# Performance work log

Measured on AMD Instinct MI355X. Metric: run time of the kernel, lower is better.

Reference implementation:

```python
import jax, jax.numpy as jnp
import numpy as np

GROUPS = 32
EPS = 1e-6


def group_norm(h, scale, bias):
    B, C, H, W = h.shape
    hg = h.reshape(B, GROUPS, -1)
    mu = hg.mean(axis=-1, keepdims=True)
    var = hg.var(axis=-1, keepdims=True)
    hg = (hg - mu) * jax.lax.rsqrt(var + EPS)
    h = hg.reshape(B, C, H, W)
    return h * scale[None, :, None, None] + bias[None, :, None, None]


def conv1x1(h, W, b):
    # 1x1 conv == per-pixel linear: (B,C,H,W) x (O,C) -> (B,O,H,W)
    return jnp.einsum('bchw,oc->bohw', h, W) + b[None, :, None, None]


def setup_inputs() -> dict:
    key = jax.random.key(0)
    ks = jax.random.split(key, 6)
    B, C, H, W = 8, 512, 64, 64
    s = 0.02
    return {
        'x': jax.random.normal(ks[0], (B, C, H, W), jnp.float32),
        'gn_scale': jnp.ones((C,), jnp.float32),
        'gn_bias': jnp.zeros((C,), jnp.float32),
        'Wq': jax.random.normal(ks[1], (C, C), jnp.float32) * s,
        'bq': jnp.zeros((C,), jnp.float32),
        'Wk': jax.random.normal(ks[2], (C, C), jnp.float32) * s,
        'bk': jnp.zeros((C,), jnp.float32),
        'Wv': jax.random.normal(ks[3], (C, C), jnp.float32) * s,
        'bv': jnp.zeros((C,), jnp.float32),
        'Wo': jax.random.normal(ks[4], (C, C), jnp.float32) * s,
        'bo': jnp.zeros((C,), jnp.float32),
    }


def reference(x, gn_scale, gn_bias, Wq, bq, Wk, bk, Wv, bv, Wo, bo):
    B, C, H, W = x.shape
    N = H * W
    h = group_norm(x, gn_scale, gn_bias)
    q = conv1x1(h, Wq, bq).reshape(B, C, N)   # (B,C,N)
    k = conv1x1(h, Wk, bk).reshape(B, C, N)
    v = conv1x1(h, Wv, bv).reshape(B, C, N)
    # scores: q^T k, scaled by C^-0.5
    w = jnp.einsum('bcq,bck->bqk', q, k) * (C ** -0.5)  # (B,N_q,N_k)
    w = jax.nn.softmax(w, axis=-1)
    # h = v @ w^T  -> (B,C,N_q)
    h = jnp.einsum('bck,bqk->bcq', v, w).reshape(B, C, H, W)
    h = conv1x1(h, Wo, bo)
    return x + h
```

## Files before the change

kernel.cpp:

```cpp
#include <hip/hip_runtime.h>
#include <math.h>

typedef __bf16 bf16_t;
typedef __bf16 bf8v __attribute__((ext_vector_type(8)));
typedef __bf16 bf4v __attribute__((ext_vector_type(4)));
typedef float  f4v  __attribute__((ext_vector_type(4)));

#define BB  8
#define CC  512
#define NN  4096
#define CPG 16
#define NCb (NN * CC)
#define WSZ (CC * CC)

#define FLG_SIZES 805306368.f
#define FLG_WS    536870912.f

__global__ void diag_out(float* out, float v) { if (threadIdx.x == 0) out[0] = v; }

__device__ __forceinline__ void gload_lds16(const bf16_t* g, bf16_t* l)
{
    __builtin_amdgcn_global_load_lds(
        (const __attribute__((address_space(1))) unsigned int*)g,
        (__attribute__((address_space(3))) unsigned int*)l, 16, 0, 0);
}

__global__ __launch_bounds__(256) void cvt_w(const float* __restrict__ a,
                                             const float* __restrict__ b,
                                             const float* __restrict__ c,
                                             const float* __restrict__ d,
                                             bf16_t* __restrict__ o)
{
    const int i = (blockIdx.x * 256 + threadIdx.x) * 4;
    const float* srcs[4] = {a, b, c, d};
#pragma unroll
    for (int m = 0; m < 4; m++) {
        float4 v = *(const float4*)(srcs[m] + i);
        bf4v w;
        w[0] = (bf16_t)v.x; w[1] = (bf16_t)v.y;
        w[2] = (bf16_t)v.z; w[3] = (bf16_t)v.w;
        *(bf4v*)(o + (size_t)m * WSZ + i) = w;
    }
}

__global__ __launch_bounds__(256) void gn_stats_part(const float* __restrict__ x,
                                                     double* __restrict__ part)
{
    const int bg = blockIdx.x >> 2;
    const int sl = blockIdx.x & 3;
    const int tid = threadIdx.x;
    const float4* xv = (const float4*)(x + (size_t)bg * CPG * NN) + sl * 4096;
    double s[4] = {0, 0, 0, 0}, ss[4] = {0, 0, 0, 0};
#pragma unroll
    for (int ii = 0; ii < 16; ii++) {
        float4 v = xv[tid + ii * 256];
        const int a = ii & 3;
        s[a]  += (double)v.x + (double)v.y + (double)v.z + (double)v.w;
        ss[a] += (double)v.x * v.x + (double)v.y * v.y
               + (double)v.z * v.z + (double)v.w * v.w;
    }
    double sT = s[0] + s[1] + s[2] + s[3];
    double ssT = ss[0] + ss[1] + ss[2] + ss[3];
    __shared__ double l1[256], l2[256];
    l1[tid] = sT; l2[tid] = ssT;
    __syncthreads();
    for (int o = 128; o > 0; o >>= 1) {
        if (tid < o) { l1[tid] += l1[tid + o]; l2[tid] += l2[tid + o]; }
        __syncthreads();
    }
    if (tid == 0) {
        part[(size_t)blockIdx.x * 2]     = l1[0];
        part[(size_t)blockIdx.x * 2 + 1] = l2[0];
    }
}

__global__ __launch_bounds__(256) void gn_stats_fin(const double* __restrict__ part,
                                                    float* __restrict__ stats)
{
    const int bg = threadIdx.x;
    double s = 0.0, ss = 0.0;
#pragma unroll
    for (int sl = 0; sl < 4; sl++) {
        s  += part[(size_t)(bg * 4 + sl) * 2];
        ss += part[(size_t)(bg * 4 + sl) * 2 + 1];
    }
    double mean = s * (1.0 / 65536.0);
    double var  = ss * (1.0 / 65536.0) - mean * mean;
    stats[bg * 2]     = (float)mean;
    stats[bg * 2 + 1] = (float)(1.0 / sqrt(var + 1e-6));
}

__global__ __launch_bounds__(256) void gn_apply_all(const float* __restrict__ x,
                                                    const float* __restrict__ gw,
                                                    const float* __restrict__ gb,
                                                    const float* __restrict__ stats,
                                                    bf16_t* __restrict__ h_all)
{
    const int b  = blockIdx.y;
    const int g  = blockIdx.x >> 4;
    const int sl = blockIdx.x & 15;
    const float* xp = x + (size_t)b * CC * NN + (size_t)g * CPG * NN;
    bf16_t* h = h_all + (size_t)b * NCb;
    const int tid = threadIdx.x;
    const float mean = stats[(b * 32 + g) * 2];
    const float rstd = stats[(b * 32 + g) * 2 + 1];
    const int cw = tid & 15;
    const float aa = rstd * gw[g * CPG + cw];
    const float bb = gb[g * CPG + cw] - mean * aa;

    __shared__ float tile[CPG][260];
    const int n0 = sl * 256;
    for (int i = tid; i < (CPG * 256) / 4; i += 256) {
        int c  = i >> 6;
        int n4 = i & 63;
        float4 v = *(const float4*)(xp + (size_t)c * NN + n0 + n4 * 4);
        tile[c][n4 * 4 + 0] = v.x;
        tile[c][n4 * 4 + 1] = v.y;
        tile[c][n4 * 4 + 2] = v.z;
        tile[c][n4 * 4 + 3] = v.w;
    }
    __syncthreads();
#pragma unroll
    for (int j = 0; j < 16; j++) {
        int n = (tid >> 4) + 16 * j;
        float v = tile[cw][n] * aa + bb;
        h[(size_t)(n0 + n) * CC + g * CPG + cw] = (bf16_t)v;
    }
}

__global__ __launch_bounds__(256) void gn_apply(const float* __restrict__ xb,
                                                const float* __restrict__ gw,
                                                const float* __restrict__ gb,
                                                const float* __restrict__ stats,
                                                bf16_t* __restrict__ h,
                                                int bg0)
{
    const int g  = blockIdx.x >> 4;
    const int sl = blockIdx.x & 15;
    const float* xp = xb + (size_t)g * CPG * NN;
    const int tid = threadIdx.x;
    const float mean = stats[(bg0 + g) * 2];
    const float rstd = stats[(bg0 + g) * 2 + 1];
    const int cw = tid & 15;
    const float aa = rstd * gw[g * CPG + cw];
    const float bb = gb[g * CPG + cw] - mean * aa;

    __shared__ float tile[CPG][260];
    const int n0 = sl * 256;
    for (int i = tid; i < (CPG * 256) / 4; i += 256) {
        int c  = i >> 6;
        int n4 = i & 63;
        float4 v = *(const float4*)(xp + (size_t)c * NN + n0 + n4 * 4);
        tile[c][n4 * 4 + 0] = v.x;
        tile[c][n4 * 4 + 1] = v.y;
        tile[c][n4 * 4 + 2] = v.z;
        tile[c][n4 * 4 + 3] = v.w;
    }
    __syncthreads();
#pragma unroll
    for (int j = 0; j < 16; j++) {
        int n = (tid >> 4) + 16 * j;
        float v = tile[cw][n] * aa + bb;
        h[(size_t)(n0 + n) * CC + g * CPG + cw] = (bf16_t)v;
    }
}

#define ABUF (128 * 32)
#define BBUF (256 * 32)

__device__ __forceinline__ void gemm_core_w(
    const bf16_t* __restrict__ A, const bf16_t* __restrict__ B,
    int K, int lda, int ldb, size_t m0, size_t n0,
    bf16_t* Asm, bf16_t* Bsm,
    int wave, int lane, int wm, int wn, int fr, int fq, f4v acc[4][8])
{
    const int gr = lane >> 2;
    const int gc = (lane & 3) << 3;
    const bf16_t* pa = A + (m0 + wave * 32 + gr) * lda + gc;
    const bf16_t* pb = B + (n0 + wave * 64 + gr) * ldb + gc;
    const int la0 = (wave * 32) * 32;
    const int lb0 = (wave * 64) * 32;

    {
        bf16_t* lA = Asm + la0;
        bf16_t* lB = Bsm + lb0;
        gload_lds16(pa,                     lA);
        gload_lds16(pa + (size_t)16 * lda,  lA + 16 * 32);
        gload_lds16(pb,                     lB);
        gload_lds16(pb + (size_t)16 * ldb,  lB + 16 * 32);
        gload_lds16(pb + (size_t)32 * ldb,  lB + 32 * 32);
        gload_lds16(pb + (size_t)48 * ldb,  lB + 48 * 32);
    }

    int buf = 0;
    for (int kt = 0; kt < K; kt += 32) {
        if (kt + 32 < K) {
            const int nb = buf ^ 1;
            bf16_t* lA = Asm + nb * ABUF + la0;
            bf16_t* lB = Bsm + nb * BBUF + lb0;
            const int kn = kt + 32;
            gload_lds16(pa + kn,                     lA);
            gload_lds16(pa + kn + (size_t)16 * lda,  lA + 16 * 32);
            gload_lds16(pb + kn,                     lB);
            gload_lds16(pb + kn + (size_t)16 * ldb,  lB + 16 * 32);
            gload_lds16(pb + kn + (size_t)32 * ldb,  lB + 32 * 32);
            gload_lds16(pb + kn + (size_t)48 * ldb,  lB + 48 * 32);
            asm volatile("s_waitcnt vmcnt(6)" ::: "memory");
        } else {
            asm volatile("s_waitcnt vmcnt(0)" ::: "memory");
        }
        __builtin_amdgcn_s_barrier();

        const bf16_t* As = Asm + buf * ABUF;
        const bf16_t* Bs = Bsm + buf * BBUF;
        bf8v af[4], bfv[8];
#pragma unroll
        for (int j = 0; j < 8; j++)
            bfv[j] = *(const bf8v*)(Bs + (wn + j * 16 + fr) * 32 + fq * 8);
#pragma unroll
        for (int i = 0; i < 4; i++)
            af[i] = *(const bf8v*)(As + (wm + i * 16 + fr) * 32 + fq * 8);
#pragma unroll
        for (int i = 0; i < 4; i++)
#pragma unroll
            for (int j = 0; j < 8; j++)
                acc[i][j] = __builtin_amdgcn_mfma_f32_16x16x32_bf16(
                    af[i], bfv[j], acc[i][j], 0, 0, 0);

        __builtin_amdgcn_s_barrier();
        buf ^= 1;
    }
}

template <int MODE>
__global__ __launch_bounds__(256, 2) void gemm_bt(
    const bf16_t* __restrict__ A, const bf16_t* __restrict__ B,
    void* __restrict__ Og, const float* __restrict__ bias,
    const float* __restrict__ resid, float scale,
    int K, int lda, int ldb, int ldo)
{
    __shared__ bf16_t Asm[2 * ABUF];
    __shared__ bf16_t Bsm[2 * BBUF];
    const int tid  = threadIdx.x;
    const int lane = tid & 63, wave = tid >> 6;
    const int wm = (wave >> 1) << 6, wn = (wave & 1) << 7;
    const int fr = lane & 15, fq = lane >> 4;
    const size_t m0 = (size_t)blockIdx.x * 128, n0 = (size_t)blockIdx.y * 256;

    f4v acc[4][8];
#pragma unroll
    for (int i = 0; i < 4; i++)
#pragma unroll
        for (int j = 0; j < 8; j++) acc[i][j] = (f4v){0.f, 0.f, 0.f, 0.f};

    gemm_core_w(A, B, K, lda, ldb, m0, n0, Asm, Bsm,
                wave, lane, wm, wn, fr, fq, acc);

    if (MODE == 0) {
        bf16_t* out = (bf16_t*)Og;
#pragma unroll
        for (int i = 0; i < 4; i++) {
            const int mb = (int)m0 + wm + i * 16 + fq * 4;
#pragma unroll
            for (int j = 0; j < 8; j++) {
                const int n = (int)n0 + wn + j * 16 + fr;
                const float bn = bias ? bias[n] : 0.f;
#pragma unroll
                for (int t = 0; t < 4; t++)
                    out[(size_t)(mb + t) * ldo + n] =
                        (bf16_t)(acc[i][j][t] * scale + bn);
            }
        }
    } else {
        float* out = (float*)Og;
#pragma unroll
        for (int i = 0; i < 4; i++) {
            const int mb = (int)m0 + wm + i * 16 + fq * 4;
#pragma unroll
            for (int j = 0; j < 8; j++) {
                const int n = (int)n0 + wn + j * 16 + fr;
                const float bn = bias[n];
                float4 rq = *(const float4*)(resid + (size_t)n * ldo + mb);
                float4 o4;
                o4.x = acc[i][j][0] * scale + bn + rq.x;
                o4.y = acc[i][j][1] * scale + bn + rq.y;
                o4.z = acc[i][j][2] * scale + bn + rq.z;
                o4.w = acc[i][j][3] * scale + bn + rq.w;
                *(float4*)(out + (size_t)n * ldo + mb) = o4;
            }
        }
    }
}

__global__ __launch_bounds__(256, 2) void gemm_qkt(
    const bf16_t* __restrict__ q_all, const bf16_t* __restrict__ k_all,
    bf16_t* __restrict__ S2, int bp, float scale)
{
    __shared__ bf16_t Asm[2 * ABUF];
    __shared__ bf16_t Bsm[2 * BBUF];
    const int z = blockIdx.z;
    const bf16_t* A = q_all + (size_t)(bp + z) * NCb;
    const bf16_t* B = k_all + (size_t)(bp + z) * NCb;
    bf16_t* out = S2 + (size_t)z * NN * NN;

    const int tid  = threadIdx.x;
    const int lane = tid & 63, wave = tid >> 6;
    const int wm = (wave >> 1) << 6, wn = (wave & 1) << 7;
    const int fr = lane & 15, fq = lane >> 4;
    const size_t m0 = (size_t)blockIdx.x * 128, n0 = (size_t)blockIdx.y * 256;

    f4v acc[4][8];
#pragma unroll
    for (int i = 0; i < 4; i++)
#pragma unroll
        for (int j = 0; j < 8; j++) acc[i][j] = (f4v){0.f, 0.f, 0.f, 0.f};

    gemm_core_w(A, B, 512, 512, 512, m0, n0, Asm, Bsm,
                wave, lane, wm, wn, fr, fq, acc);

#pragma unroll
    for (int i = 0; i < 4; i++) {
        const int mb = (int)m0 + wm + i * 16 + fq * 4;
#pragma unroll
        for (int j = 0; j < 8; j++) {
            const int n = (int)n0 + wn + j * 16 + fr;
#pragma unroll
            for (int t = 0; t < 4; t++)
                out[(size_t)(mb + t) * NN + n] = (bf16_t)(acc[i][j][t] * scale);
        }
    }
}

__global__ __launch_bounds__(256, 2) void gemm_pv2(
    const bf16_t* __restrict__ S2, const bf16_t* __restrict__ v_all,
    float* __restrict__ P, int bp)
{
    __shared__ bf16_t Asm[2 * ABUF];
    __shared__ bf16_t Bsm[2 * BBUF];
    const int slot = blockIdx.z >> 2;
    const int s    = blockIdx.z & 3;
    const int k0   = s * 1024;
    const bf16_t* A = S2 + (size_t)slot * NN * NN + k0;
    const bf16_t* B = v_all + (size_t)(bp + slot) * NCb + k0;
    float* out = P + ((size_t)slot * 4 + s) * NCb;

    const int tid  = threadIdx.x;
    const int lane = tid & 63, wave = tid >> 6;
    const int wm = (wave >> 1) << 6, wn = (wave & 1) << 7;
    const int fr = lane & 15, fq = lane >> 4;
    const size_t m0 = (size_t)blockIdx.x * 128, n0 = (size_t)blockIdx.y * 256;

    f4v acc[4][8];
#pragma unroll
    for (int i = 0; i < 4; i++)
#pragma unroll
        for (int j = 0; j < 8; j++) acc[i][j] = (f4v){0.f, 0.f, 0.f, 0.f};

    gemm_core_w(A, B, 1024, NN, NN, m0, n0, Asm, Bsm,
                wave, lane, wm, wn, fr, fq, acc);

#pragma unroll
    for (int i = 0; i < 4; i++) {
        const int mb = (int)m0 + wm + i * 16 + fq * 4;
#pragma unroll
        for (int j = 0; j < 8; j++) {
            const int n = (int)n0 + wn + j * 16 + fr;
#pragma unroll
            for (int t = 0; t < 4; t++)
                out[(size_t)(mb + t) * CC + n] = acc[i][j][t];
        }
    }
}

__global__ __launch_bounds__(256) void pv_reduce2(const float* __restrict__ P,
                                                  bf16_t* __restrict__ O_all,
                                                  int bp)
{
    const int slot = blockIdx.y;
    const size_t i = ((size_t)blockIdx.x * 256 + threadIdx.x) * 4;
    const float* Ps = P + (size_t)slot * 4 * NCb;
    float4 sv = *(const float4*)(Ps + i);
#pragma unroll
    for (int z = 1; z < 4; z++) {
        float4 t = *(const float4*)(Ps + (size_t)z * NCb + i);
        sv.x += t.x; sv.y += t.y; sv.z += t.z; sv.w += t.w;
    }
    bf4v o;
    o[0] = (bf16_t)sv.x; o[1] = (bf16_t)sv.y;
    o[2] = (bf16_t)sv.z; o[3] = (bf16_t)sv.w;
    *(bf4v*)(O_all + (size_t)(bp + slot) * NCb + i) = o;
}

__global__ __launch_bounds__(256, 2) void gemm_pv_split(
    const bf16_t* __restrict__ A, const bf16_t* __restrict__ B,
    float* __restrict__ P, int KS)
{
    __shared__ bf16_t Asm[2 * ABUF];
    __shared__ bf16_t Bsm[2 * BBUF];
    const int tid  = threadIdx.x;
    const int lane = tid & 63, wave = tid >> 6;
    const int wm = (wave >> 1) << 6, wn = (wave & 1) << 7;
    const int fr = lane & 15, fq = lane >> 4;
    const size_t m0 = (size_t)blockIdx.x * 128, n0 = (size_t)blockIdx.y * 256;
    const int z  = blockIdx.z;
    const int k0 = z * KS;

    f4v acc[4][8];
#pragma unroll
    for (int i = 0; i < 4; i++)
#pragma unroll
        for (int j = 0; j < 8; j++) acc[i][j] = (f4v){0.f, 0.f, 0.f, 0.f};

    gemm_core_w(A + k0, B + k0, KS, NN, NN, m0, n0, Asm, Bsm,
                wave, lane, wm, wn, fr, fq, acc);

    float* out = P + (size_t)z * NCb;
#pragma unroll
    for (int i = 0; i < 4; i++) {
        const int mb = (int)m0 + wm + i * 16 + fq * 4;
#pragma unroll
        for (int j = 0; j < 8; j++) {
            const int n = (int)n0 + wn + j * 16 + fr;
#pragma unroll
            for (int t = 0; t < 4; t++)
                out[(size_t)(mb + t) * CC + n] = acc[i][j][t];
        }
    }
}

__global__ __launch_bounds__(256) void pv_reduce(const float* __restrict__ P,
                                                 bf16_t* __restrict__ O, int NS)
{
    const size_t i = ((size_t)blockIdx.x * 256 + threadIdx.x) * 4;
    float4 s = *(const float4*)(P + i);
    for (int z = 1; z < NS; z++) {
        float4 t = *(const float4*)(P + (size_t)z * NCb + i);
        s.x += t.x; s.y += t.y; s.z += t.z; s.w += t.w;
    }
    bf4v o;
    o[0] = (bf16_t)s.x; o[1] = (bf16_t)s.y;
    o[2] = (bf16_t)s.z; o[3] = (bf16_t)s.w;
    *(bf4v*)(O + i) = o;
}

__global__ __launch_bounds__(256, 2) void gemm_out_all(
    const bf16_t* __restrict__ Oall, const bf16_t* __restrict__ Wo,
    float* __restrict__ outg, const float* __restrict__ bo,
    const float* __restrict__ x)
{
    __shared__ bf16_t Asm[2 * ABUF];
    __shared__ bf16_t Bsm[2 * BBUF];
    const int b = blockIdx.z;
    const bf16_t* A = Oall + (size_t)b * NCb;
    float* out = outg + (size_t)b * CC * NN;
    const float* resid = x + (size_t)b * CC * NN;

    const int tid  = threadIdx.x;
    const int lane = tid & 63, wave = tid >> 6;
    const int wm = (wave >> 1) << 6, wn = (wave & 1) << 7;
    const int fr = lane & 15, fq = lane >> 4;
    const size_t m0 = (size_t)blockIdx.x * 128, n0 = (size_t)blockIdx.y * 256;

    f4v acc[4][8];
#pragma unroll
    for (int i = 0; i < 4; i++)
#pragma unroll
        for (int j = 0; j < 8; j++) acc[i][j] = (f4v){0.f, 0.f, 0.f, 0.f};

    gemm_core_w(A, Wo, 512, 512, 512, m0, n0, Asm, Bsm,
                wave, lane, wm, wn, fr, fq, acc);

#pragma unroll
    for (int i = 0; i < 4; i++) {
        const int mb = (int)m0 + wm + i * 16 + fq * 4;
#pragma unroll
        for (int j = 0; j < 8; j++) {
            const int n = (int)n0 + wn + j * 16 + fr;
            const float bn = bo[n];
            float4 rq = *(const float4*)(resid + (size_t)n * NN + mb);
            float4 o4;
            o4.x = acc[i][j][0] + bn + rq.x;
            o4.y = acc[i][j][1] + bn + rq.y;
            o4.z = acc[i][j][2] + bn + rq.z;
            o4.w = acc[i][j][3] + bn + rq.w;
            *(float4*)(out + (size_t)n * NN + mb) = o4;
        }
    }
}

__global__ __launch_bounds__(256, 2) void gemm_qkv_all(
    const bf16_t* __restrict__ h_all, const bf16_t* __restrict__ Wb,
    const float* __restrict__ bq, const float* __restrict__ bk,
    const float* __restrict__ bv,
    bf16_t* __restrict__ q_all, bf16_t* __restrict__ k_all,
    bf16_t* __restrict__ v_all)
{
    __shared__ bf16_t Asm[2 * ABUF];
    __shared__ bf16_t Bsm[2 * BBUF];
    const int sel = blockIdx.z >> 3;
    const int b   = blockIdx.z & 7;
    const bf16_t* h = h_all + (size_t)b * NCb;
    const bf16_t* B = Wb + (size_t)sel * WSZ;
    const float* bias = (sel == 0) ? bq : (sel == 1) ? bk : bv;
    bf16_t* out = ((sel == 0) ? q_all : (sel == 1) ? k_all : v_all)
                + (size_t)b * NCb;

    const int tid  = threadIdx.x;
    const int lane = tid & 63, wave = tid >> 6;
    const int wm = (wave >> 1) << 6, wn = (wave & 1) << 7;
    const int fr = lane & 15, fq = lane >> 4;
    const size_t m0 = (size_t)blockIdx.x * 128, n0 = (size_t)blockIdx.y * 256;

    f4v acc[4][8];
#pragma unroll
    for (int i = 0; i < 4; i++)
#pragma unroll
        for (int j = 0; j < 8; j++) acc[i][j] = (f4v){0.f, 0.f, 0.f, 0.f};

    gemm_core_w(h, B, 512, 512, 512, m0, n0, Asm, Bsm,
                wave, lane, wm, wn, fr, fq, acc);

    if (sel < 2) {
#pragma unroll
        for (int i = 0; i < 4; i++) {
            const int mb = (int)m0 + wm + i * 16 + fq * 4;
#pragma unroll
            for (int j = 0; j < 8; j++) {
                const int n = (int)n0 + wn + j * 16 + fr;
                const float bn = bias[n];
#pragma unroll
                for (int t = 0; t < 4; t++)
                    out[(size_t)(mb + t) * 512 + n] =
                        (bf16_t)(acc[i][j][t] + bn);
            }
        }
    } else {
#pragma unroll
        for (int i = 0; i < 4; i++) {
            const int mb = (int)m0 + wm + i * 16 + fq * 4;
#pragma unroll
            for (int j = 0; j < 8; j++) {
                const int n = (int)n0 + wn + j * 16 + fr;
                const float bn = bias[n];
                bf4v pk;
#pragma unroll
                for (int t = 0; t < 4; t++)
                    pk[t] = (bf16_t)(acc[i][j][t] + bn);
                *(bf4v*)(out + (size_t)n * NN + mb) = pk;
            }
        }
    }
}

__global__ __launch_bounds__(256, 2) void gemm_qkv(
    const bf16_t* __restrict__ h, const bf16_t* __restrict__ Wb,
    const float* __restrict__ bq, const float* __restrict__ bk,
    const float* __restrict__ bv,
    bf16_t* __restrict__ q, bf16_t* __restrict__ k, bf16_t* __restrict__ v)
{
    __shared__ bf16_t Asm[2 * ABUF];
    __shared__ bf16_t Bsm[2 * BBUF];
    const int z = blockIdx.z;
    const bf16_t* B = Wb + (size_t)z * WSZ;
    const float* bias = (z == 0) ? bq : (z == 1) ? bk : bv;
    bf16_t* out = (z == 0) ? q : (z == 1) ? k : v;

    const int tid  = threadIdx.x;
    const int lane = tid & 63, wave = tid >> 6;
    const int wm = (wave >> 1) << 6, wn = (wave & 1) << 7;
    const int fr = lane & 15, fq = lane >> 4;
    const size_t m0 = (size_t)blockIdx.x * 128, n0 = (size_t)blockIdx.y * 256;

    f4v acc[4][8];
#pragma unroll
    for (int i = 0; i < 4; i++)
#pragma unroll
        for (int j = 0; j < 8; j++) acc[i][j] = (f4v){0.f, 0.f, 0.f, 0.f};

    gemm_core_w(h, B, 512, 512, 512, m0, n0, Asm, Bsm,
                wave, lane, wm, wn, fr, fq, acc);

    if (z < 2) {
#pragma unroll
        for (int i = 0; i < 4; i++) {
            const int mb = (int)m0 + wm + i * 16 + fq * 4;
#pragma unroll
            for (int j = 0; j < 8; j++) {
                const int n = (int)n0 + wn + j * 16 + fr;
                const float bn = bias[n];
#pragma unroll
                for (int t = 0; t < 4; t++)
                    out[(size_t)(mb + t) * 512 + n] =
                        (bf16_t)(acc[i][j][t] + bn);
            }
        }
    } else {
#pragma unroll
        for (int i = 0; i < 4; i++) {
            const int mb = (int)m0 + wm + i * 16 + fq * 4;
#pragma unroll
            for (int j = 0; j < 8; j++) {
                const int n = (int)n0 + wn + j * 16 + fr;
                const float bn = bias[n];
                bf4v pk;
#pragma unroll
                for (int t = 0; t < 4; t++)
                    pk[t] = (bf16_t)(acc[i][j][t] + bn);
                *(bf4v*)(out + (size_t)n * NN + mb) = pk;
            }
        }
    }
}

__global__ __launch_bounds__(256) void softmax_kernel(bf16_t* __restrict__ S)
{
    const int wave = threadIdx.x >> 6, lane = threadIdx.x & 63;
    const size_t row = (size_t)blockIdx.x * 4 + wave;
    bf16_t* p = S + row * NN;
    float f[64];
    float mx = -1e30f;
#pragma unroll
    for (int c = 0; c < 8; c++) {
        bf8v v = ((const bf8v*)p)[c * 64 + lane];
#pragma unroll
        for (int j = 0; j < 8; j++) {
            f[c * 8 + j] = (float)v[j];
            mx = fmaxf(mx, f[c * 8 + j]);
        }
    }
#pragma unroll
    for (int off = 32; off > 0; off >>= 1) mx = fmaxf(mx, __shfl_xor(mx, off));
    float sum = 0.f;
#pragma unroll
    for (int i = 0; i < 64; i++) { f[i] = expf(f[i] - mx); sum += f[i]; }
#pragma unroll
    for (int off = 32; off > 0; off >>= 1) sum += __shfl_xor(sum, off);
    const float inv = 1.f / sum;
#pragma unroll
    for (int c = 0; c < 8; c++) {
        bf8v o;
#pragma unroll
        for (int j = 0; j < 8; j++) o[j] = (bf16_t)(f[c * 8 + j] * inv);
        ((bf8v*)p)[c * 64 + lane] = o;
    }
}

extern "C" void kernel_launch(void* const* d_in, const int* in_sizes, int n_in,
                              void* d_out, int out_size, void* d_ws, size_t ws_size,
                              hipStream_t stream)
{
    const float* x  = (const float*)d_in[0];
    const float* gw = (const float*)d_in[1];
    const float* gb = (const float*)d_in[2];
    const float* Wq = (const float*)d_in[3];
    const float* bq = (const float*)d_in[4];
    const float* Wk = (const float*)d_in[5];
    const float* bk = (const float*)d_in[6];
    const float* Wv = (const float*)d_in[7];
    const float* bv = (const float*)d_in[8];
    const float* Wo = (const float*)d_in[9];
    const float* bo = (const float*)d_in[10];
    float* out = (float*)d_out;

    bool ok = (n_in == 11) && (out_size == BB * CC * NN) &&
              (in_sizes[0] == BB * CC * NN) &&
              (in_sizes[1] == CC) && (in_sizes[2] == CC) &&
              (in_sizes[3] == WSZ) && (in_sizes[4] == CC) &&
              (in_sizes[5] == WSZ) && (in_sizes[6] == CC) &&
              (in_sizes[7] == WSZ) && (in_sizes[8] == CC) &&
              (in_sizes[9] == WSZ) && (in_sizes[10] == CC);
    if (!ok) { diag_out<<<dim3(1), 64, 0, stream>>>(out, FLG_SIZES); return; }

    const float sc = 0.044194173824159216f;

    bf16_t* Wb    = (bf16_t*)d_ws;
    float*  stats = (float*)(Wb + (size_t)4 * WSZ);
    double* part  = (double*)(stats + 1024);
    bf16_t* base  = (bf16_t*)(part + 2048);
    const size_t head = (size_t)4 * WSZ * 2 + 1024 * 4 + 2048 * 8;

    const size_t sfull = (size_t)NN * NN * 2;

    cvt_w<<<dim3(256), 256, 0, stream>>>(Wq, Wk, Wv, Wo, Wb);
    gn_stats_part<<<dim3(1024), 256, 0, stream>>>(x, part);
    gn_stats_fin<<<dim3(1), 256, 0, stream>>>(part, stats);

    if (ws_size >= head + (size_t)4 * BB * NCb * 2 + 2 * sfull) {
        bf16_t* h_all = base;
        bf16_t* q_all = h_all + (size_t)BB * NCb;
        bf16_t* k_all = q_all + (size_t)BB * NCb;
        bf16_t* v_all = k_all + (size_t)BB * NCb;
        bf16_t* S2    = v_all + (size_t)BB * NCb;
        float*  P     = out;
        bf16_t* O_all = h_all;

        gn_apply_all<<<dim3(512, 8), 256, 0, stream>>>(x, gw, gb, stats, h_all);
        gemm_qkv_all<<<dim3(32, 2, 24), 256, 0, stream>>>(
            h_all, Wb, bq, bk, bv, q_all, k_all, v_all);

        for (int bp = 0; bp < BB; bp += 2) {
            gemm_qkt<<<dim3(32, 16, 2), 256, 0, stream>>>(
                q_all, k_all, S2, bp, sc);
            softmax_kernel<<<dim3(2 * NN / 4), 256, 0, stream>>>(S2);
            gemm_pv2<<<dim3(32, 2, 8), 256, 0, stream>>>(S2, v_all, P, bp);
            pv_reduce2<<<dim3(NCb / 1024, 2), 256, 0, stream>>>(P, O_all, bp);
        }

        gemm_out_all<<<dim3(32, 2, 8), 256, 0, stream>>>(
            O_all, Wb + (size_t)3 * WSZ, out, bo, x);
        return;
    }

    bf16_t* h = base;
    bf16_t* q = h + (size_t)NCb;
    bf16_t* k = q + (size_t)NCb;
    bf16_t* v = k + (size_t)NCb;
    bf16_t* S = v + (size_t)NCb;
    bf16_t* O = h;
    const size_t fixed = head + (size_t)4 * NCb * 2;

    if (ws_size < fixed + (size_t)128 * NN * 2) {
        diag_out<<<dim3(1), 64, 0, stream>>>(out, FLG_WS); return;
    }

    int NS = 0;
    if (ws_size >= fixed + sfull + (size_t)8 * NCb * 4)      NS = 8;
    else if (ws_size >= fixed + sfull + (size_t)4 * NCb * 4) NS = 4;
    else if (ws_size >= fixed + sfull + (size_t)2 * NCb * 4) NS = 2;

    if (NS) {
        float* P = (float*)(S + (size_t)NN * NN);
        for (int b = 0; b < BB; b++) {
            const float* xb   = x   + (size_t)b * CC * NN;
            float*       outb = out + (size_t)b * CC * NN;

            gn_apply<<<dim3(512), 256, 0, stream>>>(xb, gw, gb, stats, h, b * 32);
            gemm_qkv<<<dim3(32, 2, 3), 256, 0, stream>>>(h, Wb, bq, bk, bv, q, k, v);

            gemm_bt<0><<<dim3(32, 16), 256, 0, stream>>>(
                q, k, S, nullptr, nullptr, sc, 512, 512, 512, 4096);
            softmax_kernel<<<dim3(NN / 4), 256, 0, stream>>>(S);

            gemm_pv_split<<<dim3(32, 2, NS), 256, 0, stream>>>(S, v, P, NN / NS);
            pv_reduce<<<dim3(NCb / 1024), 256, 0, stream>>>(P, O, NS);

            gemm_bt<2><<<dim3(32, 2), 256, 0, stream>>>(
                O, Wb + (size_t)3 * WSZ, outb, bo, xb, 1.f,
                512, 512, 512, 4096);
        }
        return;
    }

    int CH = 128;
    while (CH < NN && fixed + (size_t)(CH * 2) * NN * 2 <= ws_size) CH *= 2;

    for (int b = 0; b < BB; b++) {
        const float* xb   = x   + (size_t)b * CC * NN;
        float*       outb = out + (size_t)b * CC * NN;

        gn_apply<<<dim3(512), 256, 0, stream>>>(xb, gw, gb, stats, h, b * 32);
        gemm_qkv<<<dim3(32, 2, 3), 256, 0, stream>>>(h, Wb, bq, bk, bv, q, k, v);

        for (int r0 = 0; r0 < NN; r0 += CH) {
            gemm_bt<0><<<dim3(CH / 128, 16), 256, 0, stream>>>(
                q + (size_t)r0 * CC, k, S, nullptr, nullptr, sc,
                512, 512, 512, 4096);
            softmax_kernel<<<dim3(CH / 4), 256, 0, stream>>>(S);
            gemm_bt<0><<<dim3(CH / 128, 2), 256, 0, stream>>>(
                S, v, O + (size_t)r0 * CC, nullptr, nullptr, 1.f,
                4096, 4096, 4096, 512);
        }

        gemm_bt<2><<<dim3(32, 2), 256, 0, stream>>>(
            O, Wb + (size_t)3 * WSZ, outb, bo, xb, 1.f,
            512, 512, 512, 4096);
    }
}
```

Before: 806.7 us.

## Triple-buffer GEMM LDS pipeline and XOR-swizzle LDS layout

Moves the shared GEMM core from double to triple buffering, so two K-tiles of global-to-LDS loads are in flight, with vmcnt waits adjusted to match. It also XOR-swizzles the 16-byte column chunk per row on both the global source address and the LDS fragment reads to reduce LDS bank conflicts. LDS per block grows from 48 KB to 72 KB, which may cut occupancy below the two blocks per CU requested in launch bounds.

```diff
diff --git a/kernel.cpp b/kernel.cpp
--- a/kernel.cpp
+++ b/kernel.cpp
@@ -167,6 +167,19 @@
 
 #define ABUF (128 * 32)
 #define BBUF (256 * 32)
+#define NBUF 3
+
+__device__ __forceinline__ void stage_tile(
+    const bf16_t* pa, const bf16_t* pb, int lda, int ldb,
+    bf16_t* lA, bf16_t* lB)
+{
+    gload_lds16(pa,                     lA);
+    gload_lds16(pa + (size_t)16 * lda,  lA + 16 * 32);
+    gload_lds16(pb,                     lB);
+    gload_lds16(pb + (size_t)16 * ldb,  lB + 16 * 32);
+    gload_lds16(pb + (size_t)32 * ldb,  lB + 32 * 32);
+    gload_lds16(pb + (size_t)48 * ldb,  lB + 48 * 32);
+}
 
 __device__ __forceinline__ void gemm_core_w(
     const bf16_t* __restrict__ A, const bf16_t* __restrict__ B,
@@ -174,37 +187,27 @@
     bf16_t* Asm, bf16_t* Bsm,
     int wave, int lane, int wm, int wn, int fr, int fq, f4v acc[4][8])
 {
-    const int gr = lane >> 2;
-    const int gc = (lane & 3) << 3;
-    const bf16_t* pa = A + (m0 + wave * 32 + gr) * lda + gc;
-    const bf16_t* pb = B + (n0 + wave * 64 + gr) * ldb + gc;
+    const int gr  = lane >> 2;
+    const int gcs = (((lane & 3) ^ (gr & 3)) << 3);
+    const bf16_t* pa = A + (m0 + wave * 32 + gr) * lda + gcs;
+    const bf16_t* pb = B + (n0 + wave * 64 + gr) * ldb + gcs;
     const int la0 = (wave * 32) * 32;
     const int lb0 = (wave * 64) * 32;
-
-    {
-        bf16_t* lA = Asm + la0;
-        bf16_t* lB = Bsm + lb0;
-        gload_lds16(pa,                     lA);
-        gload_lds16(pa + (size_t)16 * lda,  lA + 16 * 32);
-        gload_lds16(pb,                     lB);
-        gload_lds16(pb + (size_t)16 * ldb,  lB + 16 * 32);
-        gload_lds16(pb + (size_t)32 * ldb,  lB + 32 * 32);
-        gload_lds16(pb + (size_t)48 * ldb,  lB + 48 * 32);
-    }
+    const int fqs = ((fq ^ (fr & 3)) << 3);
+
+    stage_tile(pa, pb, lda, ldb, Asm + la0, Bsm + lb0);
+    if (K > 32)
+        stage_tile(pa + 32, pb + 32, lda, ldb,
+                   Asm + ABUF + la0, Bsm + BBUF + lb0);
 
     int buf = 0;
     for (int kt = 0; kt < K; kt += 32) {
-        if (kt + 32 < K) {
-            const int nb = buf ^ 1;
-            bf16_t* lA = Asm + nb * ABUF + la0;
-            bf16_t* lB = Bsm + nb * BBUF + lb0;
-            const int kn = kt + 32;
-            gload_lds16(pa + kn,                     lA);
-            gload_lds16(pa + kn + (size_t)16 * lda,  lA + 16 * 32);
-            gload_lds16(pb + kn,                     lB);
-            gload_lds16(pb + kn + (size_t)16 * ldb,  lB + 16 * 32);
-            gload_lds16(pb + kn + (size_t)32 * ldb,  lB + 32 * 32);
-            gload_lds16(pb + kn + (size_t)48 * ldb,  lB + 48 * 32);
+        if (kt + 64 < K) {
+            const int nb = (buf + 2 >= NBUF) ? buf + 2 - NBUF : buf + 2;
+            stage_tile(pa + kt + 64, pb + kt + 64, lda, ldb,
+                       Asm + nb * ABUF + la0, Bsm + nb * BBUF + lb0);
+            asm volatile("s_waitcnt vmcnt(12)" ::: "memory");
+        } else if (kt + 32 < K) {
             asm volatile("s_waitcnt vmcnt(6)" ::: "memory");
         } else {
             asm volatile("s_waitcnt vmcnt(0)" ::: "memory");
@@ -216,10 +219,10 @@
         bf8v af[4], bfv[8];
 #pragma unroll
         for (int j = 0; j < 8; j++)
-            bfv[j] = *(const bf8v*)(Bs + (wn + j * 16 + fr) * 32 + fq * 8);
+            bfv[j] = *(const bf8v*)(Bs + (wn + j * 16 + fr) * 32 + fqs);
 #pragma unroll
         for (int i = 0; i < 4; i++)
-            af[i] = *(const bf8v*)(As + (wm + i * 16 + fr) * 32 + fq * 8);
+            af[i] = *(const bf8v*)(As + (wm + i * 16 + fr) * 32 + fqs);
 #pragma unroll
         for (int i = 0; i < 4; i++)
 #pragma unroll
@@ -228,7 +231,7 @@
                     af[i], bfv[j], acc[i][j], 0, 0, 0);
 
         __builtin_amdgcn_s_barrier();
-        buf ^= 1;
+        buf = (buf + 1 == NBUF) ? 0 : buf + 1;
     }
 }
 
@@ -239,8 +242,8 @@
     const float* __restrict__ resid, float scale,
     int K, int lda, int ldb, int ldo)
 {
-    __shared__ bf16_t Asm[2 * ABUF];
-    __shared__ bf16_t Bsm[2 * BBUF];
+    __shared__ bf16_t Asm[NBUF * ABUF];
+    __shared__ bf16_t Bsm[NBUF * BBUF];
     const int tid  = threadIdx.x;
     const int lane = tid & 63, wave = tid >> 6;
     const int wm = (wave >> 1) << 6, wn = (wave & 1) << 7;
@@ -296,8 +299,8 @@
     const bf16_t* __restrict__ q_all, const bf16_t* __restrict__ k_all,
     bf16_t* __restrict__ S2, int bp, float scale)
 {
-    __shared__ bf16_t Asm[2 * ABUF];
-    __shared__ bf16_t Bsm[2 * BBUF];
+    __shared__ bf16_t Asm[NBUF * ABUF];
+    __shared__ bf16_t Bsm[NBUF * BBUF];
     const int z = blockIdx.z;
     const bf16_t* A = q_all + (size_t)(bp + z) * NCb;
     const bf16_t* B = k_all + (size_t)(bp + z) * NCb;
@@ -335,8 +338,8 @@
     const bf16_t* __restrict__ S2, const bf16_t* __restrict__ v_all,
     float* __restrict__ P, int bp)
 {
-    __shared__ bf16_t Asm[2 * ABUF];
-    __shared__ bf16_t Bsm[2 * BBUF];
+    __shared__ bf16_t Asm[NBUF * ABUF];
+    __shared__ bf16_t Bsm[NBUF * BBUF];
     const int slot = blockIdx.z >> 2;
     const int s    = blockIdx.z & 3;
     const int k0   = s * 1024;
@@ -395,8 +398,8 @@
     const bf16_t* __restrict__ A, const bf16_t* __restrict__ B,
     float* __restrict__ P, int KS)
 {
-    __shared__ bf16_t Asm[2 * ABUF];
-    __shared__ bf16_t Bsm[2 * BBUF];
+    __shared__ bf16_t Asm[NBUF * ABUF];
+    __shared__ bf16_t Bsm[NBUF * BBUF];
     const int tid  = threadIdx.x;
     const int lane = tid & 63, wave = tid >> 6;
     const int wm = (wave >> 1) << 6, wn = (wave & 1) << 7;
@@ -448,8 +451,8 @@
     float* __restrict__ outg, const float* __restrict__ bo,
     const float* __restrict__ x)
 {
-    __shared__ bf16_t Asm[2 * ABUF];
-    __shared__ bf16_t Bsm[2 * BBUF];
+    __shared__ bf16_t Asm[NBUF * ABUF];
+    __shared__ bf16_t Bsm[NBUF * BBUF];
     const int b = blockIdx.z;
     const bf16_t* A = Oall + (size_t)b * NCb;
     float* out = outg + (size_t)b * CC * NN;
@@ -495,8 +498,8 @@
     bf16_t* __restrict__ q_all, bf16_t* __restrict__ k_all,
     bf16_t* __restrict__ v_all)
 {
-    __shared__ bf16_t Asm[2 * ABUF];
-    __shared__ bf16_t Bsm[2 * BBUF];
+    __shared__ bf16_t Asm[NBUF * ABUF];
+    __shared__ bf16_t Bsm[NBUF * BBUF];
     const int sel = blockIdx.z >> 3;
     const int b   = blockIdx.z & 7;
     const bf16_t* h = h_all + (size_t)b * NCb;
@@ -558,8 +561,8 @@
     const float* __restrict__ bv,
     bf16_t* __restrict__ q, bf16_t* __restrict__ k, bf16_t* __restrict__ v)
 {
-    __shared__ bf16_t Asm[2 * ABUF];
-    __shared__ bf16_t Bsm[2 * BBUF];
+    __shared__ bf16_t Asm[NBUF * ABUF];
+    __shared__ bf16_t Bsm[NBUF * BBUF];
     const int z = blockIdx.z;
     const bf16_t* B = Wb + (size_t)z * WSZ;
     const float* bias = (z == 0) ? bq : (z == 1) ? bk : bv;
```

Result: no change. 811.0 us (+0.5%).
